# Kernel tuning notes

Hardware: AMD Instinct MI355X
Metric: run time of the kernel (lower is better)

Reference implementation:

```python
import jax
import jax.numpy as jnp
from jax import lax
import numpy as np

IN_SCALE, IN_ZP = 0.01, 7
W_SCALE, W_ZP = 0.01, 3
B_SCALE = 0.0001
I32_MIN, I32_MAX = -(2.0**31), 2.0**31 - 1


def setup_inputs() -> dict:
    key = jax.random.key(0)
    k1, k2, k3 = jax.random.split(key, 3)
    # int8 quantized input activations and weights (torch passes torch.int8 tensors)
    inputVec = jax.random.randint(k1, (32, 128, 56, 56), -128, 128, dtype=jnp.int32).astype(jnp.int8)
    weight = jax.random.randint(k2, (256, 128, 3, 3), -128, 128, dtype=jnp.int32).astype(jnp.int8)
    bias = jax.random.normal(k3, (256,), dtype=jnp.float32)
    return {"inputVec": inputVec, "weight": weight, "bias": bias}


def reference(inputVec, weight, bias):
    # dequantize per-tensor: (q - zero_point) * scale
    x = (inputVec.astype(jnp.float32) - IN_ZP) * IN_SCALE   # [N, Cin, H, W]
    w = (weight.astype(jnp.float32) - W_ZP) * W_SCALE       # [Cout, Cin, kh, kw]
    # quantize bias to qint32 (round-half-even, clamp to int32 range) then dequantize
    b = jnp.clip(jnp.round(bias / B_SCALE), I32_MIN, I32_MAX) * B_SCALE  # [Cout]
    # conv2d: stride 1, no padding, dilation 1, groups 1
    out = lax.conv_general_dilated(
        x, w,
        window_strides=(1, 1),
        padding='VALID',
        dimension_numbers=('NCHW', 'OIHW', 'NCHW'),
    )  # [N, Cout, H-2, W-2]
    return out + b[None, :, None, None]
```

## Files before the change

### kernel.cpp

```cpp
#include <hip/hip_runtime.h>
#include <hip/hip_bf16.h>


#define N_B   32
#define C_IN  128
#define H_IN  56
#define W_IN  56
#define C_OUT 256
#define H_OUT 54
#define W_OUT 54
#define K_TOT 1152
#define NPX   (N_B * H_OUT * W_OUT)
#define PXROW (H_OUT * W_OUT)

using i32x4  = __attribute__((ext_vector_type(4))) int;

static __device__ __forceinline__ int dot4(int a, int b, int c) {
#if __has_builtin(__builtin_amdgcn_sdot4)
  return __builtin_amdgcn_sdot4(a, b, c, false);
#else
  signed char a0 = (signed char)a, a1 = (signed char)(a >> 8),
              a2 = (signed char)(a >> 16), a3 = (signed char)(a >> 24);
  signed char b0 = (signed char)b, b1 = (signed char)(b >> 8),
              b2 = (signed char)(b >> 16), b3 = (signed char)(b >> 24);
  return c + a0 * b0 + a1 * b1 + a2 * b2 + a3 * b3;
#endif
}

__device__ __forceinline__ void gload16(const void* g, void* l) {
  __builtin_amdgcn_global_load_lds(
      (const __attribute__((address_space(1))) void*)g,
      (__attribute__((address_space(3))) void*)l, 16, 0, 0);
}

__global__ void prep(const int* __restrict__ in, const int* __restrict__ wsrc,
                     const float* __restrict__ bias,
                     signed char* __restrict__ ip2, int* __restrict__ rs,
                     signed char* __restrict__ wq3, float* __restrict__ bconst) {
  const int bid = blockIdx.x, tid = threadIdx.x;
  __shared__ int t32[C_IN * W_IN];
  __shared__ int rsum[W_IN];

  if (bid < 1792) {
    const int h = bid % 56, n = bid / 56;
    if (tid < W_IN) rsum[tid] = 0;
    int ci = tid >> 1, hf = tid & 1;
    const int* s = in + ((size_t)n * C_IN + ci) * (H_IN * W_IN) + h * W_IN + hf * 28;
    int* d = &t32[ci * W_IN + hf * 28];
#pragma unroll
    for (int k = 0; k < 7; ++k)
      *(int4*)(d + k * 4) = *(const int4*)(s + k * 4);
    __syncthreads();

    signed char* dst = ip2 + ((size_t)n * H_IN + h) * 8192;
#pragma unroll
    for (int jj = 0; jj < 2; ++jj) {
      int j = jj * 256 + tid;
      int q = j >> 6, w = j & 63;
      if (w < W_IN) {
        int b[4], srow = 0;
#pragma unroll
        for (int qq = 0; qq < 4; ++qq) {
          int x0 = t32[(q * 16 + qq * 4 + 0) * W_IN + w];
          int x1 = t32[(q * 16 + qq * 4 + 1) * W_IN + w];
          int x2 = t32[(q * 16 + qq * 4 + 2) * W_IN + w];
          int x3 = t32[(q * 16 + qq * 4 + 3) * W_IN + w];
          b[qq] = (x0 & 255) | ((x1 & 255) << 8) | ((x2 & 255) << 16) | ((x3 & 255) << 24);
          srow = dot4(b[qq], 0x01010101, srow);
        }
        *(int4*)(dst + (size_t)q * 1024 + w * 16) = *(int4*)b;
        atomicAdd(&rsum[w], srow);
      }
    }
    __syncthreads();
    if (tid < W_IN) rs[((size_t)n * H_IN + h) * W_IN + tid] = rsum[tid];
  } else {
    int* red = t32;
    const int co = (bid - 1792) * 2 + (tid >> 7);
    const int ci = tid & 127;
    const int* wrow = wsrc + (size_t)co * K_TOT + (size_t)ci * 9;
    int s = 0;
    int kk = ci >> 5, hh = (ci >> 4) & 1, b = ci & 15;
    size_t base = (size_t)kk * 8192 + hh * 4096 + co * 16 + b;
#pragma unroll
    for (int t = 0; t < 9; ++t) {
      int v = wrow[t];
      s += v;
      wq3[(size_t)t * 32768 + base] = (signed char)v;
    }
    red[tid] = s;
    __syncthreads();
    for (int off = 64; off > 0; off >>= 1) {
      if (ci < off) red[tid] += red[tid + off];
      __syncthreads();
    }
    if (ci == 0) {
      int wsum = red[tid];
      float r = rintf(bias[co] / 0.0001f);
      r = fminf(fmaxf(r, -2147483648.0f), 2147483647.0f);
      bconst[co] = 1e-4f * (float)(-7 * wsum + 24192) + r * 0.0001f;
    }
  }
}

__device__ __forceinline__ int mklb(int pf, int pxl, int c16) {
  int j = pf * 16 + pxl;
  int jc = j > 107 ? 107 : j;
  int dy = (jc >= 54) ? 1 : 0;
  return c16 * 4096 + dy * 1024 + (jc - dy * 54) * 16;
}

__launch_bounds__(256, 4)
__global__ void conv_mfma(const signed char* __restrict__ ip2,
                          const signed char* __restrict__ wq3,
                          const int* __restrict__ rs,
                          const float* __restrict__ bconst,
                          float* __restrict__ out) {
  __shared__ signed char lds[32768];
  __shared__ float asf_lds[112];
  const int tid = threadIdx.x, w = tid >> 6, l = tid & 63;
  const int c16 = l >> 4, pxl = l & 15;

  const int b0 = blockIdx.x;
  const int wg = (b0 & 7) * 216 + (b0 >> 3);
  const int cq = wg & 1;
  const int nr = wg >> 1;
  const int n  = nr / 27;
  const int rp = nr - n * 27;
  const int y0 = rp * 2;

  const signed char* ipn = ip2 + ((size_t)n * H_IN + y0) * 8192;
  {
    const int r = tid >> 6;
    const int off = (tid & 63) * 16;
    const signed char* src = ipn + (size_t)r * 8192 + off;
#pragma unroll
    for (int i = 0; i < 8; ++i)
      gload16(src + (size_t)i * 1024, &lds[i * 4096 + tid * 16]);
  }

  if (tid < 108) {
    int dy = (tid >= 54) ? 1 : 0;
    int x  = tid - dy * 54;
    const int* rp_ = rs + ((size_t)n * H_IN + y0 + dy) * W_IN + x;
    int s = 0;
#pragma unroll
    for (int kh = 0; kh < 3; ++kh)
      s += rp_[kh * W_IN + 0] + rp_[kh * W_IN + 1] + rp_[kh * W_IN + 2];
    asf_lds[tid] = -3e-4f * (float)s;
  }

  const int lb0 = mklb(0, pxl, c16), lb1 = mklb(1, pxl, c16), lb2 = mklb(2, pxl, c16),
            lb3 = mklb(3, pxl, c16), lb4 = mklb(4, pxl, c16), lb5 = mklb(5, pxl, c16),
            lb6 = mklb(6, pxl, c16);

  const signed char* awq = wq3 + (size_t)c16 * 4096 +
                           (size_t)(cq * 128 + w * 32 + pxl) * 16;

  i32x4 a0_0 = {0,0,0,0}, a0_1 = {0,0,0,0}, a0_2 = {0,0,0,0}, a0_3 = {0,0,0,0},
        a0_4 = {0,0,0,0}, a0_5 = {0,0,0,0}, a0_6 = {0,0,0,0};
  i32x4 a1_0 = {0,0,0,0}, a1_1 = {0,0,0,0}, a1_2 = {0,0,0,0}, a1_3 = {0,0,0,0},
        a1_4 = {0,0,0,0}, a1_5 = {0,0,0,0}, a1_6 = {0,0,0,0};
  i32x4 wa0, wa1, wb0, wb1;

#define LDW(P, t)                                                              \
  P##0 = *(const i32x4*)(awq + (size_t)(t) * 16384);                           \
  P##1 = *(const i32x4*)(awq + (size_t)(t) * 16384 + 256);

  LDW(wa, 0);
  __syncthreads();

#define KSTEP(ks, U, L, DOLOAD)                                                \
  {                                                                            \
    if (DOLOAD) { LDW(L, (ks) + 1); }                                          \
    __builtin_amdgcn_sched_barrier(0);                                         \
    constexpr int d_ = ((ks) & 1) * 16384 + (((ks) >> 1) / 3) * 1024 +         \
                       (((ks) >> 1) % 3) * 16;                                 \
    {                                                                          \
      i32x4 q0 = *(const i32x4*)(&lds[lb0 + d_]);                              \
      i32x4 q1 = *(const i32x4*)(&lds[lb1 + d_]);                              \
      i32x4 q2 = *(const i32x4*)(&lds[lb2 + d_]);                              \
      i32x4 q3 = *(const i32x4*)(&lds[lb3 + d_]);                              \
      __builtin_amdgcn_s_setprio(1);                                           \
      a0_0 = __builtin_amdgcn_mfma_i32_16x16x64_i8(U##0, q0, a0_0, 0, 0, 0);   \
      a1_0 = __builtin_amdgcn_mfma_i32_16x16x64_i8(U##1, q0, a1_0, 0, 0, 0);   \
      a0_1 = __builtin_amdgcn_mfma_i32_16x16x64_i8(U##0, q1, a0_1, 0, 0, 0);   \
      a1_1 = __builtin_amdgcn_mfma_i32_16x16x64_i8(U##1, q1, a1_1, 0, 0, 0);   \
      a0_2 = __builtin_amdgcn_mfma_i32_16x16x64_i8(U##0, q2, a0_2, 0, 0, 0);   \
      a1_2 = __builtin_amdgcn_mfma_i32_16x16x64_i8(U##1, q2, a1_2, 0, 0, 0);   \
      a0_3 = __builtin_amdgcn_mfma_i32_16x16x64_i8(U##0, q3, a0_3, 0, 0, 0);   \
      a1_3 = __builtin_amdgcn_mfma_i32_16x16x64_i8(U##1, q3, a1_3, 0, 0, 0);   \
      __builtin_amdgcn_s_setprio(0);                                           \
    }                                                                          \
    __builtin_amdgcn_sched_barrier(0);                                         \
    {                                                                          \
      i32x4 q4 = *(const i32x4*)(&lds[lb4 + d_]);                              \
      i32x4 q5 = *(const i32x4*)(&lds[lb5 + d_]);                              \
      i32x4 q6 = *(const i32x4*)(&lds[lb6 + d_]);                              \
      __builtin_amdgcn_s_setprio(1);                                           \
      a0_4 = __builtin_amdgcn_mfma_i32_16x16x64_i8(U##0, q4, a0_4, 0, 0, 0);   \
      a1_4 = __builtin_amdgcn_mfma_i32_16x16x64_i8(U##1, q4, a1_4, 0, 0, 0);   \
      a0_5 = __builtin_amdgcn_mfma_i32_16x16x64_i8(U##0, q5, a0_5, 0, 0, 0);   \
      a1_5 = __builtin_amdgcn_mfma_i32_16x16x64_i8(U##1, q5, a1_5, 0, 0, 0);   \
      a0_6 = __builtin_amdgcn_mfma_i32_16x16x64_i8(U##0, q6, a0_6, 0, 0, 0);   \
      a1_6 = __builtin_amdgcn_mfma_i32_16x16x64_i8(U##1, q6, a1_6, 0, 0, 0);   \
      __builtin_amdgcn_s_setprio(0);                                           \
    }                                                                          \
  }

  KSTEP(0,  wa, wb, 1)  KSTEP(1,  wb, wa, 1)  KSTEP(2,  wa, wb, 1)
  KSTEP(3,  wb, wa, 1)  KSTEP(4,  wa, wb, 1)  KSTEP(5,  wb, wa, 1)
  KSTEP(6,  wa, wb, 1)  KSTEP(7,  wb, wa, 1)  KSTEP(8,  wa, wb, 1)
  KSTEP(9,  wb, wa, 1)  KSTEP(10, wa, wb, 1)  KSTEP(11, wb, wa, 1)
  KSTEP(12, wa, wb, 1)  KSTEP(13, wb, wa, 1)  KSTEP(14, wa, wb, 1)
  KSTEP(15, wb, wa, 1)  KSTEP(16, wa, wb, 1)  KSTEP(17, wb, wa, 0)
#undef KSTEP
#undef LDW

  float* obase = out + ((size_t)n * C_OUT + cq * 128) * PXROW + y0 * W_OUT;
  const float asf0 = asf_lds[pxl];
  const float asf1 = asf_lds[16 + pxl];
  const float asf2 = asf_lds[32 + pxl];
  const float asf3 = asf_lds[48 + pxl];
  const float asf4 = asf_lds[64 + pxl];
  const float asf5 = asf_lds[80 + pxl];
  const int j6 = 96 + pxl;
  const float asf6 = (j6 < 108) ? asf_lds[j6] : 0.0f;
#pragma unroll
  for (int m = 0; m < 2; ++m) {
#pragma unroll
    for (int j = 0; j < 4; ++j) {
      int co = w * 32 + m * 16 + c16 * 4 + j;
      float bc = bconst[cq * 128 + co];
      float* o = obase + (size_t)co * PXROW;
      const i32x4& v0 = m ? a1_0 : a0_0;
      const i32x4& v1 = m ? a1_1 : a0_1;
      const i32x4& v2 = m ? a1_2 : a0_2;
      const i32x4& v3 = m ? a1_3 : a0_3;
      const i32x4& v4 = m ? a1_4 : a0_4;
      const i32x4& v5 = m ? a1_5 : a0_5;
      const i32x4& v6 = m ? a1_6 : a0_6;
      o[pxl]      = 1e-4f * (float)v0[j] + asf0 + bc;
      o[16 + pxl] = 1e-4f * (float)v1[j] + asf1 + bc;
      o[32 + pxl] = 1e-4f * (float)v2[j] + asf2 + bc;
      o[48 + pxl] = 1e-4f * (float)v3[j] + asf3 + bc;
      o[64 + pxl] = 1e-4f * (float)v4[j] + asf4 + bc;
      o[80 + pxl] = 1e-4f * (float)v5[j] + asf5 + bc;
      if (j6 < 108)
        o[j6] = 1e-4f * (float)v6[j] + asf6 + bc;
    }
  }
}

__global__ void conv_naive(const int* __restrict__ in, const int* __restrict__ w,
                           const float* __restrict__ bias, float* __restrict__ out) {
  size_t idx = (size_t)blockIdx.x * 256 + threadIdx.x;
  size_t total = (size_t)N_B * C_OUT * H_OUT * W_OUT;
  if (idx >= total) return;
  int x = idx % W_OUT; size_t t = idx / W_OUT;
  int y = t % H_OUT; t /= H_OUT;
  int co = t % C_OUT; int n = (int)(t / C_OUT);
  int acc = 0;
  for (int ci = 0; ci < C_IN; ++ci) {
    const int* ib = in + (((size_t)n * C_IN + ci) * H_IN + y) * W_IN + x;
    const int* wb = w + (((size_t)co * C_IN + ci) * 3) * 3;
    for (int kh = 0; kh < 3; ++kh)
      for (int kw = 0; kw < 3; ++kw)
        acc += (ib[kh * W_IN + kw] - 7) * (wb[kh * 3 + kw] - 3);
  }
  float r = rintf(bias[co] / 0.0001f);
  r = fminf(fmaxf(r, -2147483648.0f), 2147483647.0f);
  out[idx] = (float)acc * (0.01f * 0.01f) + r * 0.0001f;
}

extern "C" void kernel_launch(void* const* d_in, const int* in_sizes, int n_in,
                              void* d_out, int out_size, void* d_ws, size_t ws_size,
                              hipStream_t stream) {
  const int*   in   = (const int*)d_in[0];
  const int*   w    = (const int*)d_in[1];
  const float* bias = (const float*)d_in[2];
  float*       out  = (float*)d_out;

  const size_t WQ_OFF = 0;
  const size_t IP_OFF = 294912;
  const size_t RS_OFF = IP_OFF + 14680064;
  const size_t BC_OFF = RS_OFF + 401408;
  const size_t NEED   = BC_OFF + 1024;

  if (ws_size >= NEED) {
    char* ws = (char*)d_ws;
    signed char* wq3  = (signed char*)(ws + WQ_OFF);
    signed char* ip2  = (signed char*)(ws + IP_OFF);
    int*         rs   = (int*)(ws + RS_OFF);
    float*       bc   = (float*)(ws + BC_OFF);

    prep<<<1920, 256, 0, stream>>>(in, w, bias, ip2, rs, wq3, bc);
    conv_mfma<<<1728, 256, 0, stream>>>(ip2, wq3, rs, bc, out);
  } else {
    size_t total = (size_t)N_B * C_OUT * H_OUT * W_OUT;
    conv_naive<<<(total + 255) / 256, 256, 0, stream>>>(in, w, bias, out);
  }
}
```

Baseline: 50.48 us.

## Retile conv to one output row by all 256 output channels per block

```diff
diff --git a/kernel.cpp b/kernel.cpp
--- a/kernel.cpp
+++ b/kernel.cpp
@@ -103,46 +103,32 @@
   }
 }
 
-__device__ __forceinline__ int mklb(int pf, int pxl, int c16) {
-  int j = pf * 16 + pxl;
-  int jc = j > 107 ? 107 : j;
-  int dy = (jc >= 54) ? 1 : 0;
-  return c16 * 4096 + dy * 1024 + (jc - dy * 54) * 16;
-}
-
 __launch_bounds__(256, 4)
 __global__ void conv_mfma(const signed char* __restrict__ ip2,
                           const signed char* __restrict__ wq3,
                           const int* __restrict__ rs,
                           const float* __restrict__ bconst,
                           float* __restrict__ out) {
-  __shared__ signed char lds[32768];
-  __shared__ float asf_lds[112];
-  const int tid = threadIdx.x, w = tid >> 6, l = tid & 63;
+  __shared__ signed char lds[24576];
+  __shared__ float asf_lds[54];
+  const int tid = threadIdx.x, wv = tid >> 6, l = tid & 63;
   const int c16 = l >> 4, pxl = l & 15;
 
   const int b0 = blockIdx.x;
   const int wg = (b0 & 7) * 216 + (b0 >> 3);
-  const int cq = wg & 1;
-  const int nr = wg >> 1;
-  const int n  = nr / 27;
-  const int rp = nr - n * 27;
-  const int y0 = rp * 2;
-
-  const signed char* ipn = ip2 + ((size_t)n * H_IN + y0) * 8192;
-  {
-    const int r = tid >> 6;
-    const int off = (tid & 63) * 16;
-    const signed char* src = ipn + (size_t)r * 8192 + off;
-#pragma unroll
-    for (int i = 0; i < 8; ++i)
-      gload16(src + (size_t)i * 1024, &lds[i * 4096 + tid * 16]);
-  }
-
-  if (tid < 108) {
-    int dy = (tid >= 54) ? 1 : 0;
-    int x  = tid - dy * 54;
-    const int* rp_ = rs + ((size_t)n * H_IN + y0 + dy) * W_IN + x;
+  const int n  = wg / 54;
+  const int y  = wg - n * 54;
+
+  const signed char* ipn = ip2 + ((size_t)n * H_IN + y) * 8192;
+#pragma unroll
+  for (int i = 0; i < 6; ++i) {
+    int s = i * 4 + wv;
+    int p = s / 3, r = s - 3 * p;
+    gload16(ipn + (size_t)r * 8192 + p * 1024 + l * 16, &lds[s * 1024 + l * 16]);
+  }
+
+  if (tid < 54) {
+    const int* rp_ = rs + ((size_t)n * H_IN + y) * W_IN + tid;
     int s = 0;
 #pragma unroll
     for (int kh = 0; kh < 3; ++kh)
@@ -150,60 +136,64 @@
     asf_lds[tid] = -3e-4f * (float)s;
   }
 
-  const int lb0 = mklb(0, pxl, c16), lb1 = mklb(1, pxl, c16), lb2 = mklb(2, pxl, c16),
-            lb3 = mklb(3, pxl, c16), lb4 = mklb(4, pxl, c16), lb5 = mklb(5, pxl, c16),
-            lb6 = mklb(6, pxl, c16);
+  const int x0c = pxl;
+  const int lb0 = c16 * 3072 + x0c * 16;
+  const int x3c = (48 + pxl > 53 ? 53 : 48 + pxl);
+  const int lb3 = c16 * 3072 + x3c * 16;
 
   const signed char* awq = wq3 + (size_t)c16 * 4096 +
-                           (size_t)(cq * 128 + w * 32 + pxl) * 16;
-
-  i32x4 a0_0 = {0,0,0,0}, a0_1 = {0,0,0,0}, a0_2 = {0,0,0,0}, a0_3 = {0,0,0,0},
-        a0_4 = {0,0,0,0}, a0_5 = {0,0,0,0}, a0_6 = {0,0,0,0};
-  i32x4 a1_0 = {0,0,0,0}, a1_1 = {0,0,0,0}, a1_2 = {0,0,0,0}, a1_3 = {0,0,0,0},
-        a1_4 = {0,0,0,0}, a1_5 = {0,0,0,0}, a1_6 = {0,0,0,0};
-  i32x4 wa0, wa1, wb0, wb1;
+                           (size_t)(wv * 64 + pxl) * 16;
+
+  i32x4 c00={0,0,0,0},c01={0,0,0,0},c02={0,0,0,0},c03={0,0,0,0},
+        c10={0,0,0,0},c11={0,0,0,0},c12={0,0,0,0},c13={0,0,0,0},
+        c20={0,0,0,0},c21={0,0,0,0},c22={0,0,0,0},c23={0,0,0,0},
+        c30={0,0,0,0},c31={0,0,0,0},c32={0,0,0,0},c33={0,0,0,0};
+  i32x4 wa0, wa1, wa2, wa3, wb0, wb1, wb2, wb3;
 
 #define LDW(P, t)                                                              \
   P##0 = *(const i32x4*)(awq + (size_t)(t) * 16384);                           \
-  P##1 = *(const i32x4*)(awq + (size_t)(t) * 16384 + 256);
+  P##1 = *(const i32x4*)(awq + (size_t)(t) * 16384 + 256);                     \
+  P##2 = *(const i32x4*)(awq + (size_t)(t) * 16384 + 512);                     \
+  P##3 = *(const i32x4*)(awq + (size_t)(t) * 16384 + 768);
 
   LDW(wa, 0);
   __syncthreads();
+
+#define SB() __builtin_amdgcn_sched_barrier(0)
 
 #define KSTEP(ks, U, L, DOLOAD)                                                \
   {                                                                            \
     if (DOLOAD) { LDW(L, (ks) + 1); }                                          \
-    __builtin_amdgcn_sched_barrier(0);                                         \
-    constexpr int d_ = ((ks) & 1) * 16384 + (((ks) >> 1) / 3) * 1024 +         \
+    SB();                                                                      \
+    constexpr int d_ = ((ks) & 1) * 12288 + (((ks) >> 1) / 3) * 1024 +         \
                        (((ks) >> 1) % 3) * 16;                                 \
     {                                                                          \
       i32x4 q0 = *(const i32x4*)(&lds[lb0 + d_]);                              \
-      i32x4 q1 = *(const i32x4*)(&lds[lb1 + d_]);                              \
-      i32x4 q2 = *(const i32x4*)(&lds[lb2 + d_]);                              \
+      i32x4 q1 = *(const i32x4*)(&lds[lb0 + 256 + d_]);                        \
+      __builtin_amdgcn_s_setprio(1);                                           \
+      c00 = __builtin_amdgcn_mfma_i32_16x16x64_i8(U##0, q0, c00, 0, 0, 0);     \
+      c10 = __builtin_amdgcn_mfma_i32_16x16x64_i8(U##1, q0, c10, 0, 0, 0);     \
+      c20 = __builtin_amdgcn_mfma_i32_16x16x64_i8(U##2, q0, c20, 0, 0, 0);     \
+      c30 = __builtin_amdgcn_mfma_i32_16x16x64_i8(U##3, q0, c30, 0, 0, 0);     \
+      c01 = __builtin_amdgcn_mfma_i32_16x16x64_i8(U##0, q1, c01, 0, 0, 0);     \
+      c11 = __builtin_amdgcn_mfma_i32_16x16x64_i8(U##1, q1, c11, 0, 0, 0);     \
+      c21 = __builtin_amdgcn_mfma_i32_16x16x64_i8(U##2, q1, c21, 0, 0, 0);     \
+      c31 = __builtin_amdgcn_mfma_i32_16x16x64_i8(U##3, q1, c31, 0, 0, 0);     \
+      __builtin_amdgcn_s_setprio(0);                                           \
+    }                                                                          \
+    SB();                                                                      \
+    {                                                                          \
+      i32x4 q2 = *(const i32x4*)(&lds[lb0 + 512 + d_]);                        \
       i32x4 q3 = *(const i32x4*)(&lds[lb3 + d_]);                              \
       __builtin_amdgcn_s_setprio(1);                                           \
-      a0_0 = __builtin_amdgcn_mfma_i32_16x16x64_i8(U##0, q0, a0_0, 0, 0, 0);   \
-      a1_0 = __builtin_amdgcn_mfma_i32_16x16x64_i8(U##1, q0, a1_0, 0, 0, 0);   \
-      a0_1 = __builtin_amdgcn_mfma_i32_16x16x64_i8(U##0, q1, a0_1, 0, 0, 0);   \
-      a1_1 = __builtin_amdgcn_mfma_i32_16x16x64_i8(U##1, q1, a1_1, 0, 0, 0);   \
-      a0_2 = __builtin_amdgcn_mfma_i32_16x16x64_i8(U##0, q2, a0_2, 0, 0, 0);   \
-      a1_2 = __builtin_amdgcn_mfma_i32_16x16x64_i8(U##1, q2, a1_2, 0, 0, 0);   \
-      a0_3 = __builtin_amdgcn_mfma_i32_16x16x64_i8(U##0, q3, a0_3, 0, 0, 0);   \
-      a1_3 = __builtin_amdgcn_mfma_i32_16x16x64_i8(U##1, q3, a1_3, 0, 0, 0);   \
-      __builtin_amdgcn_s_setprio(0);                                           \
-    }                                                                          \
-    __builtin_amdgcn_sched_barrier(0);                                         \
-    {                                                                          \
-      i32x4 q4 = *(const i32x4*)(&lds[lb4 + d_]);                              \
-      i32x4 q5 = *(const i32x4*)(&lds[lb5 + d_]);                              \
-      i32x4 q6 = *(const i32x4*)(&lds[lb6 + d_]);                              \
-      __builtin_amdgcn_s_setprio(1);                                           \
-      a0_4 = __builtin_amdgcn_mfma_i32_16x16x64_i8(U##0, q4, a0_4, 0, 0, 0);   \
-      a1_4 = __builtin_amdgcn_mfma_i32_16x16x64_i8(U##1, q4, a1_4, 0, 0, 0);   \
-      a0_5 = __builtin_amdgcn_mfma_i32_16x16x64_i8(U##0, q5, a0_5, 0, 0, 0);   \
-      a1_5 = __builtin_amdgcn_mfma_i32_16x16x64_i8(U##1, q5, a1_5, 0, 0, 0);   \
-      a0_6 = __builtin_amdgcn_mfma_i32_16x16x64_i8(U##0, q6, a0_6, 0, 0, 0);   \
-      a1_6 = __builtin_amdgcn_mfma_i32_16x16x64_i8(U##1, q6, a1_6, 0, 0, 0);   \
+      c02 = __builtin_amdgcn_mfma_i32_16x16x64_i8(U##0, q2, c02, 0, 0, 0);     \
+      c12 = __builtin_amdgcn_mfma_i32_16x16x64_i8(U##1, q2, c12, 0, 0, 0);     \
+      c22 = __builtin_amdgcn_mfma_i32_16x16x64_i8(U##2, q2, c22, 0, 0, 0);     \
+      c32 = __builtin_amdgcn_mfma_i32_16x16x64_i8(U##3, q2, c32, 0, 0, 0);     \
+      c03 = __builtin_amdgcn_mfma_i32_16x16x64_i8(U##0, q3, c03, 0, 0, 0);     \
+      c13 = __builtin_amdgcn_mfma_i32_16x16x64_i8(U##1, q3, c13, 0, 0, 0);     \
+      c23 = __builtin_amdgcn_mfma_i32_16x16x64_i8(U##2, q3, c23, 0, 0, 0);     \
+      c33 = __builtin_amdgcn_mfma_i32_16x16x64_i8(U##3, q3, c33, 0, 0, 0);     \
       __builtin_amdgcn_s_setprio(0);                                           \
     }                                                                          \
   }
@@ -216,40 +206,31 @@
   KSTEP(15, wb, wa, 1)  KSTEP(16, wa, wb, 1)  KSTEP(17, wb, wa, 0)
 #undef KSTEP
 #undef LDW
-
-  float* obase = out + ((size_t)n * C_OUT + cq * 128) * PXROW + y0 * W_OUT;
+#undef SB
+
+  float* obase = out + (size_t)n * C_OUT * PXROW + y * W_OUT;
   const float asf0 = asf_lds[pxl];
   const float asf1 = asf_lds[16 + pxl];
   const float asf2 = asf_lds[32 + pxl];
-  const float asf3 = asf_lds[48 + pxl];
-  const float asf4 = asf_lds[64 + pxl];
-  const float asf5 = asf_lds[80 + pxl];
-  const int j6 = 96 + pxl;
-  const float asf6 = (j6 < 108) ? asf_lds[j6] : 0.0f;
-#pragma unroll
-  for (int m = 0; m < 2; ++m) {
-#pragma unroll
-    for (int j = 0; j < 4; ++j) {
-      int co = w * 32 + m * 16 + c16 * 4 + j;
-      float bc = bconst[cq * 128 + co];
-      float* o = obase + (size_t)co * PXROW;
-      const i32x4& v0 = m ? a1_0 : a0_0;
-      const i32x4& v1 = m ? a1_1 : a0_1;
-      const i32x4& v2 = m ? a1_2 : a0_2;
-      const i32x4& v3 = m ? a1_3 : a0_3;
-      const i32x4& v4 = m ? a1_4 : a0_4;
-      const i32x4& v5 = m ? a1_5 : a0_5;
-      const i32x4& v6 = m ? a1_6 : a0_6;
-      o[pxl]      = 1e-4f * (float)v0[j] + asf0 + bc;
-      o[16 + pxl] = 1e-4f * (float)v1[j] + asf1 + bc;
-      o[32 + pxl] = 1e-4f * (float)v2[j] + asf2 + bc;
-      o[48 + pxl] = 1e-4f * (float)v3[j] + asf3 + bc;
-      o[64 + pxl] = 1e-4f * (float)v4[j] + asf4 + bc;
-      o[80 + pxl] = 1e-4f * (float)v5[j] + asf5 + bc;
-      if (j6 < 108)
-        o[j6] = 1e-4f * (float)v6[j] + asf6 + bc;
-    }
-  }
+  const float asf3 = (pxl < 6) ? asf_lds[48 + pxl] : 0.0f;
+
+#define STM(m, V0, V1, V2, V3)                                                 \
+  {                                                                            \
+    _Pragma("unroll") for (int j = 0; j < 4; ++j) {                            \
+      int co = wv * 64 + (m) * 16 + c16 * 4 + j;                               \
+      float bc = bconst[co];                                                   \
+      float* o = obase + (size_t)co * PXROW;                                   \
+      o[pxl]      = 1e-4f * (float)V0[j] + asf0 + bc;                          \
+      o[16 + pxl] = 1e-4f * (float)V1[j] + asf1 + bc;                          \
+      o[32 + pxl] = 1e-4f * (float)V2[j] + asf2 + bc;                          \
+      if (pxl < 6) o[48 + pxl] = 1e-4f * (float)V3[j] + asf3 + bc;             \
+    }                                                                          \
+  }
+  STM(0, c00, c01, c02, c03)
+  STM(1, c10, c11, c12, c13)
+  STM(2, c20, c21, c22, c23)
+  STM(3, c30, c31, c32, c33)
+#undef STM
 }
 
 __global__ void conv_naive(const int* __restrict__ in, const int* __restrict__ w,
```

Result: slower. 57.78 us (+14.4%).
